# Performance work log

Measured on AMD Instinct MI355X. Metric: run time of the kernel, lower is better.

## Reference

```python
import jax, jax.numpy as jnp
import numpy as np

EMBED = 256
NHEAD = 8
HDIM = EMBED // NHEAD
EPS = 1e-6


def setup_inputs() -> dict:
    key = jax.random.key(0)
    ks = jax.random.split(key, 10)
    B, L, E = 8, 8192, EMBED
    sc = 1.0 / np.sqrt(E)
    return {
        "q": jax.random.normal(ks[0], (B, L, E), jnp.float32),
        "k": jax.random.normal(ks[1], (B, L, E), jnp.float32),
        "v": jax.random.normal(ks[2], (B, L, E), jnp.float32),
        "Wq": jax.random.normal(ks[3], (E, E), jnp.float32) * sc,
        "bq": jax.random.normal(ks[4], (E,), jnp.float32) * 0.01,
        "Wk": jax.random.normal(ks[5], (E, E), jnp.float32) * sc,
        "bk": jax.random.normal(ks[6], (E,), jnp.float32) * 0.01,
        "Wv": jax.random.normal(ks[7], (E, E), jnp.float32) * sc,
        "bv": jax.random.normal(ks[8], (E,), jnp.float32) * 0.01,
        "Wm": jax.random.normal(ks[9], (E, E), jnp.float32) * sc,
    }


def _feature_map(x):
    # elu(x) + 1, the LoFTR linear-attention kernel feature map
    return jax.nn.elu(x) + 1.0


def reference(q, k, v, Wq, bq, Wk, bk, Wv, bv, Wm):
    B, L, E = q.shape
    # QKV projections (nn.Linear: x @ W.T + b), split into heads
    Q = (q @ Wq.T + bq).reshape(B, L, NHEAD, HDIM)
    K = (k @ Wk.T + bk).reshape(B, -1, NHEAD, HDIM)
    V = (v @ Wv.T + bv).reshape(B, -1, NHEAD, HDIM)

    Qf = _feature_map(Q)              # [B,L,H,D]
    Kf = _feature_map(K)              # [B,S,H,D]
    v_len = V.shape[1]
    Vn = V / v_len
    # KV: per-head outer-product accumulation over source positions
    KV = jnp.einsum("bshd,bshv->bhdv", Kf, Vn)       # [B,H,D,D]
    Ksum = Kf.sum(axis=1)                              # [B,H,D]
    Z = 1.0 / (jnp.einsum("blhd,bhd->blh", Qf, Ksum) + EPS)  # [B,L,H]
    msg = jnp.einsum("blhd,bhdv,blh->blhv", Qf, KV, Z) * v_len  # [B,L,H,D]
    # merge heads and output projection (bias=False)
    out = msg.reshape(B, L, NHEAD * HDIM) @ Wm.T
    return out
```

## Files before the change

kernel.cpp:

```cpp
#include <hip/hip_runtime.h>
#include <hip/hip_bf16.h>

#define SEQ   8192
#define NB    8
#define EMB   256
#define NHD   8
#define HDM   32
#define LDP   72

typedef __attribute__((ext_vector_type(8))) short short8;
typedef __attribute__((ext_vector_type(4))) float floatx4;
typedef __attribute__((ext_vector_type(16))) float floatx16;

__device__ __forceinline__ short f2b(float f) {
    __hip_bfloat16 h = __float2bfloat16(f);
    return __builtin_bit_cast(short, h);
}
__device__ __forceinline__ float b2f(short s) {
    unsigned u = (unsigned)(unsigned short)s << 16;
    return __builtin_bit_cast(float, u);
}

__launch_bounds__(256)
__global__ void qkv_kernel(const float* __restrict__ qin,
                           const float* __restrict__ kin,
                           const float* __restrict__ vin,
                           const float* __restrict__ Wq, const float* __restrict__ bq,
                           const float* __restrict__ Wk, const float* __restrict__ bk,
                           const float* __restrict__ Wv, const float* __restrict__ bv,
                           short* __restrict__ Qf, short* __restrict__ Kf,
                           short* __restrict__ Vn,
                           float* __restrict__ Ksum) {
    __shared__ __align__(16) short As[128 * LDP];
    __shared__ __align__(16) short Bs[128 * LDP];
    __shared__ float colsum[128];

    const int tid  = threadIdx.x;
    const int tm   = blockIdx.x;
    const int tn   = blockIdx.y;
    const int mode = blockIdx.z;
    const int lane = tid & 63;
    const int wave = tid >> 6;
    const int wm   = (wave & 1) << 6;
    const int wn   = (wave >> 1) << 6;
    const int fr   = lane & 15;
    const int fq   = lane >> 4;

    const float* X    = (mode == 0) ? qin : (mode == 1) ? kin : vin;
    const float* W    = (mode == 0) ? Wq  : (mode == 1) ? Wk  : Wv;
    const float* bias = (mode == 0) ? bq  : (mode == 1) ? bk  : bv;
    short*       out  = (mode == 0) ? Qf  : (mode == 1) ? Kf  : Vn;

    if (mode == 1 && tid < 128) colsum[tid] = 0.f;

    floatx4 acc[4][4];
    #pragma unroll
    for (int i = 0; i < 4; i++)
        #pragma unroll
        for (int j = 0; j < 4; j++)
            #pragma unroll
            for (int r = 0; r < 4; r++) acc[i][j][r] = 0.f;

    const float* Xb = X + (size_t)(tm * 128) * EMB;
    const float* Wb = W + (size_t)(tn * 128) * EMB;

    for (int kc = 0; kc < 4; kc++) {
        const int kb = kc * 64;
        #pragma unroll
        for (int u = 0; u < 8; u++) {
            const int g   = u * 256 + tid;
            const int row = g >> 4;
            const int c4  = (g & 15) * 4;
            float4 f = *(const float4*)(Xb + (size_t)row * EMB + kb + c4);
            *(short4*)&As[row * LDP + c4] =
                make_short4(f2b(f.x), f2b(f.y), f2b(f.z), f2b(f.w));
            float4 g4 = *(const float4*)(Wb + (size_t)row * EMB + kb + c4);
            *(short4*)&Bs[row * LDP + c4] =
                make_short4(f2b(g4.x), f2b(g4.y), f2b(g4.z), f2b(g4.w));
        }
        __syncthreads();
        #pragma unroll
        for (int kk = 0; kk < 64; kk += 32) {
            short8 a[4], b[4];
            #pragma unroll
            for (int i = 0; i < 4; i++)
                a[i] = *(const short8*)&As[(wm + i * 16 + fr) * LDP + kk + fq * 8];
            #pragma unroll
            for (int j = 0; j < 4; j++)
                b[j] = *(const short8*)&Bs[(wn + j * 16 + fr) * LDP + kk + fq * 8];
            #pragma unroll
            for (int i = 0; i < 4; i++)
                #pragma unroll
                for (int j = 0; j < 4; j++)
                    acc[i][j] = __builtin_amdgcn_mfma_f32_16x16x32_bf16(a[i], b[j], acc[i][j], 0, 0, 0);
        }
        __syncthreads();
    }

    const int row0 = tm * 128;
    float ks[4] = {0.f, 0.f, 0.f, 0.f};
    #pragma unroll
    for (int i = 0; i < 4; i++) {
        #pragma unroll
        for (int j = 0; j < 4; j++) {
            const int colg = tn * 128 + wn + j * 16 + fr;
            const float bia = bias[colg];
            #pragma unroll
            for (int rr = 0; rr < 4; rr++) {
                const int rowg = row0 + wm + i * 16 + fq * 4 + rr;
                float v = acc[i][j][rr] + bia;
                if (mode <= 1) v = (v > 0.f) ? (v + 1.f) : __expf(v);
                else           v *= (1.0f / (float)SEQ);
                out[(size_t)rowg * EMB + colg] = f2b(v);
                ks[j] += v;
            }
        }
    }
    if (mode == 1) {
        #pragma unroll
        for (int j = 0; j < 4; j++)
            atomicAdd(&colsum[wn + j * 16 + fr], ks[j]);
        __syncthreads();
        if (tid < 128) {
            const int b = (tm * 128) / SEQ;
            atomicAdd(&Ksum[b * EMB + tn * 128 + tid], colsum[tid]);
        }
    }
}

template <bool ATOMIC>
__launch_bounds__(256)
__global__ void kv_kernel(const short* __restrict__ Kf,
                          const short* __restrict__ Vn,
                          float* __restrict__ dst_base,
                          int kvsp) {
    __shared__ __align__(16) short Kt[32 * 256];
    __shared__ __align__(16) short Vt[32 * 256];

    const int tid  = threadIdx.x;
    const int sp   = blockIdx.x % kvsp;
    const int b    = blockIdx.x / kvsp;
    const int wave = tid >> 6;
    const int lane = tid & 63;
    const int h    = wave * 2 + (lane >> 5);
    const int l5   = lane & 31;
    const int d0   = (l5 >> 2) * 4;
    const int v0   = (l5 & 3) * 8;
    const int chunk = SEQ / kvsp;
    const size_t rowbase = (size_t)(b * SEQ + sp * chunk) * EMB;

    float acc[4][8];
    #pragma unroll
    for (int i = 0; i < 4; i++)
        #pragma unroll
        for (int j = 0; j < 8; j++) acc[i][j] = 0.f;

    for (int t0 = 0; t0 < chunk; t0 += 32) {
        __syncthreads();
        const short* ksrc = Kf + rowbase + (size_t)t0 * EMB;
        const short* vsrc = Vn + rowbase + (size_t)t0 * EMB;
        #pragma unroll
        for (int u = 0; u < 4; u++) {
            const int c   = tid + u * 256;
            const int row = c >> 5;
            const int col = (c & 31) * 8;
            *(short8*)&Kt[row * 256 + col] = *(const short8*)(ksrc + (size_t)row * EMB + col);
            *(short8*)&Vt[row * 256 + col] = *(const short8*)(vsrc + (size_t)row * EMB + col);
        }
        __syncthreads();
        #pragma unroll 4
        for (int s = 0; s < 32; s++) {
            short4 k4 = *(const short4*)&Kt[s * 256 + h * 32 + d0];
            short8 v8 = *(const short8*)&Vt[s * 256 + h * 32 + v0];
            float kf[4] = {b2f(k4.x), b2f(k4.y), b2f(k4.z), b2f(k4.w)};
            float vf[8];
            #pragma unroll
            for (int j = 0; j < 8; j++) vf[j] = b2f(v8[j]);
            #pragma unroll
            for (int i = 0; i < 4; i++)
                #pragma unroll
                for (int j = 0; j < 8; j++) acc[i][j] += kf[i] * vf[j];
        }
    }

    if (ATOMIC) {
        float* dst = dst_base + (size_t)((b * 8 + h) * 1024);
        #pragma unroll
        for (int i = 0; i < 4; i++)
            #pragma unroll
            for (int j = 0; j < 8; j++)
                atomicAdd(&dst[(d0 + i) * 32 + v0 + j], acc[i][j]);
    } else {
        float* dst = dst_base + (size_t)(((size_t)sp * NB + b) * 8 + h) * 1024;
        #pragma unroll
        for (int i = 0; i < 4; i++) {
            float4 lo = make_float4(acc[i][0], acc[i][1], acc[i][2], acc[i][3]);
            float4 hi = make_float4(acc[i][4], acc[i][5], acc[i][6], acc[i][7]);
            *(float4*)&dst[(d0 + i) * 32 + v0]     = lo;
            *(float4*)&dst[(d0 + i) * 32 + v0 + 4] = hi;
        }
    }
}

__launch_bounds__(256)
__global__ void kvred_kernel(const float* __restrict__ KVp,
                             float* __restrict__ KV, int kvsp) {
    const int i = blockIdx.x * 1024 + threadIdx.x * 4;
    float4 s = make_float4(0.f, 0.f, 0.f, 0.f);
    for (int p = 0; p < kvsp; p++) {
        float4 t = *(const float4*)&KVp[(size_t)p * 65536 + i];
        s.x += t.x; s.y += t.y; s.z += t.z; s.w += t.w;
    }
    *(float4*)&KV[i] = s;
}

__launch_bounds__(64)
__global__ void m_kernel(const float* __restrict__ KV,
                         const float* __restrict__ Wm,
                         short* __restrict__ Mt) {
    const int blk  = blockIdx.x;
    const int e0   = (blk & 7) * 32;
    const int h    = (blk >> 3) & 7;
    const int b    = blk >> 6;
    const int lane = threadIdx.x;
    const int l31  = lane & 31;
    const int q    = lane >> 5;

    floatx16 acc;
    #pragma unroll
    for (int i = 0; i < 16; i++) acc[i] = 0.f;

    #pragma unroll
    for (int kb = 0; kb < 32; kb += 16) {
        const float* ar = KV + (size_t)(((b * 8 + h) * 32 + l31) * 32) + kb + q * 8;
        const float* br = Wm + (size_t)(e0 + l31) * EMB + h * 32 + kb + q * 8;
        short8 a, w;
        #pragma unroll
        for (int t = 0; t < 8; t++) { a[t] = f2b(ar[t]); w[t] = f2b(br[t]); }
        acc = __builtin_amdgcn_mfma_f32_32x32x16_bf16(a, w, acc, 0, 0, 0);
    }

    short* mrow = Mt + (size_t)b * EMB * EMB + (size_t)(e0 + l31) * EMB + h * 32;
    #pragma unroll
    for (int r4 = 0; r4 < 4; r4++) {
        const int dbase = 8 * r4 + 4 * q;
        short4 s4 = make_short4(f2b(acc[r4 * 4 + 0]), f2b(acc[r4 * 4 + 1]),
                                f2b(acc[r4 * 4 + 2]), f2b(acc[r4 * 4 + 3]));
        *(short4*)(mrow + dbase) = s4;
    }
}

__launch_bounds__(256)
__global__ void out_kernel(const short* __restrict__ Qf,
                           const float* __restrict__ Ksum,
                           const short* __restrict__ Mt,
                           float* __restrict__ Out) {
    __shared__ __align__(16) short As[128 * LDP];
    __shared__ __align__(16) short Bs[128 * LDP];
    __shared__ float zs[128][NHD];
    __shared__ float ksl[EMB];

    const int tid  = threadIdx.x;
    const int tm   = blockIdx.x;
    const int tn   = blockIdx.y;
    const int b    = (tm * 128) / SEQ;
    const int lane = tid & 63;
    const int wave = tid >> 6;
    const int wm   = (wave & 1) << 6;
    const int wn   = (wave >> 1) << 6;
    const int fr   = lane & 15;
    const int fq   = lane >> 4;

    ksl[tid] = Ksum[b * EMB + tid];
    __syncthreads();

    {
        const int t  = tid >> 1;
        const int h0 = (tid & 1) * 4;
        const short* qrow = Qf + (size_t)(tm * 128 + t) * EMB;
        #pragma unroll
        for (int hh = 0; hh < 4; hh++) {
            const int h = h0 + hh;
            float d = 0.f;
            #pragma unroll
            for (int u = 0; u < 8; u++) {
                short4 q4 = *(const short4*)(qrow + h * 32 + 4 * u);
                d += b2f(q4.x) * ksl[h * 32 + 4 * u + 0] + b2f(q4.y) * ksl[h * 32 + 4 * u + 1]
                   + b2f(q4.z) * ksl[h * 32 + 4 * u + 2] + b2f(q4.w) * ksl[h * 32 + 4 * u + 3];
            }
            zs[t][h] = (float)SEQ / (d + 1e-6f);
        }
    }
    __syncthreads();

    floatx4 acc[4][4];
    #pragma unroll
    for (int i = 0; i < 4; i++)
        #pragma unroll
        for (int j = 0; j < 4; j++)
            #pragma unroll
            for (int r = 0; r < 4; r++) acc[i][j][r] = 0.f;

    const short* Ab = Qf + (size_t)(tm * 128) * EMB;
    const short* Bb = Mt + (size_t)b * EMB * EMB + (size_t)(tn * 128) * EMB;

    for (int kc = 0; kc < 4; kc++) {
        const int kb = kc * 64;
        #pragma unroll
        for (int u = 0; u < 4; u++) {
            const int g   = u * 256 + tid;
            const int row = g >> 3;
            const int c8  = (g & 7) * 8;
            const float z = zs[row][(kb + c8) >> 5];
            short8 qv = *(const short8*)(Ab + (size_t)row * EMB + kb + c8);
            short8 oa;
            #pragma unroll
            for (int t = 0; t < 8; t++) oa[t] = f2b(b2f(qv[t]) * z);
            *(short8*)&As[row * LDP + c8] = oa;
            *(short8*)&Bs[row * LDP + c8] = *(const short8*)(Bb + (size_t)row * EMB + kb + c8);
        }
        __syncthreads();
        #pragma unroll
        for (int kk = 0; kk < 64; kk += 32) {
            short8 a[4], bb[4];
            #pragma unroll
            for (int i = 0; i < 4; i++)
                a[i] = *(const short8*)&As[(wm + i * 16 + fr) * LDP + kk + fq * 8];
            #pragma unroll
            for (int j = 0; j < 4; j++)
                bb[j] = *(const short8*)&Bs[(wn + j * 16 + fr) * LDP + kk + fq * 8];
            #pragma unroll
            for (int i = 0; i < 4; i++)
                #pragma unroll
                for (int j = 0; j < 4; j++)
                    acc[i][j] = __builtin_amdgcn_mfma_f32_16x16x32_bf16(a[i], bb[j], acc[i][j], 0, 0, 0);
        }
        __syncthreads();
    }

    const int row0 = tm * 128;
    #pragma unroll
    for (int i = 0; i < 4; i++) {
        #pragma unroll
        for (int j = 0; j < 4; j++) {
            const int colg = tn * 128 + wn + j * 16 + fr;
            #pragma unroll
            for (int rr = 0; rr < 4; rr++) {
                const int rowg = row0 + wm + i * 16 + fq * 4 + rr;
                Out[(size_t)rowg * EMB + colg] = acc[i][j][rr];
            }
        }
    }
}

extern "C" void kernel_launch(void* const* d_in, const int* in_sizes, int n_in,
                              void* d_out, int out_size, void* d_ws, size_t ws_size,
                              hipStream_t stream) {
    (void)in_sizes; (void)n_in; (void)out_size;
    const float* q  = (const float*)d_in[0];
    const float* k  = (const float*)d_in[1];
    const float* v  = (const float*)d_in[2];
    const float* Wq = (const float*)d_in[3];
    const float* bq = (const float*)d_in[4];
    const float* Wk = (const float*)d_in[5];
    const float* bk = (const float*)d_in[6];
    const float* Wv = (const float*)d_in[7];
    const float* bv = (const float*)d_in[8];
    const float* Wm = (const float*)d_in[9];

    char* ws = (char*)d_ws;
    short* Qf   = (short*)(ws);
    short* Kf   = (short*)(ws + 33554432);
    short* Vn   = (short*)(ws + 67108864);
    float* Ksum = (float*)(ws + 100663296);
    float* KV   = (float*)(ws + 100663296 + 8192);
    short* Mt   = (short*)(ws + 100663296 + 8192 + 262144);
    const size_t kvp_off = 100663296ull + 8192 + 262144 + 1048576;
    float* KVp  = (float*)(ws + kvp_off);

    int kvsp = 0;
    if      (ws_size >= kvp_off + 64ull * 262144) kvsp = 64;
    else if (ws_size >= kvp_off + 32ull * 262144) kvsp = 32;
    else if (ws_size >= kvp_off + 16ull * 262144) kvsp = 16;

    hipMemsetAsync(ws + 100663296, 0, 8192 + 262144, stream);

    dim3 blk(256);
    qkv_kernel<<<dim3(512, 2, 3), blk, 0, stream>>>(q, k, v, Wq, bq, Wk, bk, Wv, bv,
                                                    Qf, Kf, Vn, Ksum);

    if (kvsp) {
        kv_kernel<false><<<NB * kvsp, 256, 0, stream>>>(Kf, Vn, KVp, kvsp);
        kvred_kernel<<<64, 256, 0, stream>>>(KVp, KV, kvsp);
    } else {
        kv_kernel<true><<<NB * 16, 256, 0, stream>>>(Kf, Vn, KV, 16);
    }

    m_kernel<<<512, 64, 0, stream>>>(KV, Wm, Mt);
    out_kernel<<<dim3(512, 2), blk, 0, stream>>>(Qf, Ksum, Mt, (float*)d_out);
}
```

Before: 374.7 us.

## Pre-convert QKV weights to bf16 and stage tiles via direct global-to-LDS loads

Adds a small kernel that converts Wq/Wk/Wv to bf16 once per call, into workspace memory that Mt later reuses. The QKV GEMM then loads activation (fp32) and weight (bf16) tiles straight into LDS with global_load_lds 16-byte transfers, using an XOR swizzle in place of padding to avoid bank conflicts. The fp32-to-bf16 conversion of activations moves to the LDS-read side. This removes the register round-trip and per-element conversion on the store path, but doubles LDS bytes for the A tile, repeats the conversion for each wave that reads a row, and adds one kernel launch.

```diff
diff --git a/kernel.cpp b/kernel.cpp
--- a/kernel.cpp
+++ b/kernel.cpp
@@ -21,18 +21,40 @@
     return __builtin_bit_cast(float, u);
 }
 
+__device__ __forceinline__ void gload16(const void* g, void* l) {
+    __builtin_amdgcn_global_load_lds(
+        (const __attribute__((address_space(1))) unsigned*)g,
+        (__attribute__((address_space(3))) unsigned*)l, 16, 0, 0);
+}
+
+__launch_bounds__(256)
+__global__ void wconv_kernel(const float* __restrict__ Wq,
+                             const float* __restrict__ Wk,
+                             const float* __restrict__ Wv,
+                             short* __restrict__ Wb) {
+    const float* src = (blockIdx.y == 0) ? Wq : (blockIdx.y == 1) ? Wk : Wv;
+    const int i = (blockIdx.x * 256 + threadIdx.x) * 8;
+    float4 f0 = *(const float4*)(src + i);
+    float4 f1 = *(const float4*)(src + i + 4);
+    short8 o;
+    o[0] = f2b(f0.x); o[1] = f2b(f0.y); o[2] = f2b(f0.z); o[3] = f2b(f0.w);
+    o[4] = f2b(f1.x); o[5] = f2b(f1.y); o[6] = f2b(f1.z); o[7] = f2b(f1.w);
+    *(short8*)(Wb + (size_t)blockIdx.y * 65536 + i) = o;
+}
+
 __launch_bounds__(256)
 __global__ void qkv_kernel(const float* __restrict__ qin,
                            const float* __restrict__ kin,
                            const float* __restrict__ vin,
-                           const float* __restrict__ Wq, const float* __restrict__ bq,
-                           const float* __restrict__ Wk, const float* __restrict__ bk,
-                           const float* __restrict__ Wv, const float* __restrict__ bv,
+                           const short* __restrict__ Wb,
+                           const float* __restrict__ bq,
+                           const float* __restrict__ bk,
+                           const float* __restrict__ bv,
                            short* __restrict__ Qf, short* __restrict__ Kf,
                            short* __restrict__ Vn,
                            float* __restrict__ Ksum) {
-    __shared__ __align__(16) short As[128 * LDP];
-    __shared__ __align__(16) short Bs[128 * LDP];
+    __shared__ __align__(16) float As[128 * 64];
+    __shared__ __align__(16) short Bs[128 * 64];
     __shared__ float colsum[128];
 
     const int tid  = threadIdx.x;
@@ -47,12 +69,14 @@
     const int fq   = lane >> 4;
 
     const float* X    = (mode == 0) ? qin : (mode == 1) ? kin : vin;
-    const float* W    = (mode == 0) ? Wq  : (mode == 1) ? Wk  : Wv;
     const float* bias = (mode == 0) ? bq  : (mode == 1) ? bk  : bv;
     short*       out  = (mode == 0) ? Qf  : (mode == 1) ? Kf  : Vn;
 
     if (mode == 1 && tid < 128) colsum[tid] = 0.f;
 
+    const float* Xb = X + (size_t)(tm * 128) * EMB;
+    const short* Wt = Wb + (size_t)mode * 65536 + (size_t)(tn * 128) * EMB;
+
     floatx4 acc[4][4];
     #pragma unroll
     for (int i = 0; i < 4; i++)
@@ -60,34 +84,47 @@
         for (int j = 0; j < 4; j++)
             #pragma unroll
             for (int r = 0; r < 4; r++) acc[i][j][r] = 0.f;
-
-    const float* Xb = X + (size_t)(tm * 128) * EMB;
-    const float* Wb = W + (size_t)(tn * 128) * EMB;
 
     for (int kc = 0; kc < 4; kc++) {
         const int kb = kc * 64;
         #pragma unroll
         for (int u = 0; u < 8; u++) {
-            const int g   = u * 256 + tid;
-            const int row = g >> 4;
-            const int c4  = (g & 15) * 4;
-            float4 f = *(const float4*)(Xb + (size_t)row * EMB + kb + c4);
-            *(short4*)&As[row * LDP + c4] =
-                make_short4(f2b(f.x), f2b(f.y), f2b(f.z), f2b(f.w));
-            float4 g4 = *(const float4*)(Wb + (size_t)row * EMB + kb + c4);
-            *(short4*)&Bs[row * LDP + c4] =
-                make_short4(f2b(g4.x), f2b(g4.y), f2b(g4.z), f2b(g4.w));
+            const int c   = u * 256 + tid;
+            const int row = c >> 4;
+            const int q   = c & 15;
+            const int col = (((q >> 1) ^ (row & 7)) << 3) + ((q & 1) << 2);
+            gload16(Xb + (size_t)row * EMB + kb + col, &As[c * 4]);
+        }
+        #pragma unroll
+        for (int u = 0; u < 4; u++) {
+            const int c   = u * 256 + tid;
+            const int row = c >> 3;
+            const int q   = c & 7;
+            const int col = ((q ^ (row & 7)) << 3);
+            gload16(Wt + (size_t)row * EMB + kb + col, &Bs[c * 8]);
         }
         __syncthreads();
         #pragma unroll
         for (int kk = 0; kk < 64; kk += 32) {
             short8 a[4], b[4];
             #pragma unroll
-            for (int i = 0; i < 4; i++)
-                a[i] = *(const short8*)&As[(wm + i * 16 + fr) * LDP + kk + fq * 8];
-            #pragma unroll
-            for (int j = 0; j < 4; j++)
-                b[j] = *(const short8*)&Bs[(wn + j * 16 + fr) * LDP + kk + fq * 8];
+            for (int i = 0; i < 4; i++) {
+                const int row  = wm + i * 16 + fr;
+                const int P    = (kk >> 3) + fq;
+                const int base = row * 64 + (((P ^ (row & 7)) << 3));
+                float4 x0 = *(const float4*)&As[base];
+                float4 x1 = *(const float4*)&As[base + 4];
+                short8 t;
+                t[0] = f2b(x0.x); t[1] = f2b(x0.y); t[2] = f2b(x0.z); t[3] = f2b(x0.w);
+                t[4] = f2b(x1.x); t[5] = f2b(x1.y); t[6] = f2b(x1.z); t[7] = f2b(x1.w);
+                a[i] = t;
+            }
+            #pragma unroll
+            for (int j = 0; j < 4; j++) {
+                const int row = wn + j * 16 + fr;
+                const int qB  = (kk >> 3) + fq;
+                b[j] = *(const short8*)&Bs[row * 64 + ((qB ^ (row & 7)) << 3)];
+            }
             #pragma unroll
             for (int i = 0; i < 4; i++)
                 #pragma unroll
@@ -375,6 +412,7 @@
     float* Ksum = (float*)(ws + 100663296);
     float* KV   = (float*)(ws + 100663296 + 8192);
     short* Mt   = (short*)(ws + 100663296 + 8192 + 262144);
+    short* Wb   = (short*)(ws + 100663296 + 8192 + 262144);
     const size_t kvp_off = 100663296ull + 8192 + 262144 + 1048576;
     float* KVp  = (float*)(ws + kvp_off);
 
@@ -386,7 +424,8 @@
     hipMemsetAsync(ws + 100663296, 0, 8192 + 262144, stream);
 
     dim3 blk(256);
-    qkv_kernel<<<dim3(512, 2, 3), blk, 0, stream>>>(q, k, v, Wq, bq, Wk, bk, Wv, bv,
+    wconv_kernel<<<dim3(32, 3), blk, 0, stream>>>(Wq, Wk, Wv, Wb);
+    qkv_kernel<<<dim3(512, 2, 3), blk, 0, stream>>>(q, k, v, Wb, bq, bk, bv,
                                                     Qf, Kf, Vn, Ksum);
 
     if (kvsp) {
```

New measurement: 388.9 us. +3.8%, slower.
